# Kernel optimization log

Measured on AMD Instinct MI355X. Metric: run time of the kernel, lower is better.

The kernel has to match this reference:

```python
import jax, jax.numpy as jnp
import numpy as np

B, T, C = 16, 2048, 64  # n_embd = 64


def setup_inputs() -> dict:
    key = jax.random.key(0)
    ks = jax.random.split(key, 4)
    scale = 1.0 / np.sqrt(C)
    x = jax.random.normal(ks[0], (B, T, C), dtype=jnp.float32)
    Wk = jax.random.normal(ks[1], (C, C), dtype=jnp.float32) * scale
    Wq = jax.random.normal(ks[2], (C, C), dtype=jnp.float32) * scale
    Wv = jax.random.normal(ks[3], (C, C), dtype=jnp.float32) * scale
    bk = jnp.zeros((C,), dtype=jnp.float32)
    bq = jnp.zeros((C,), dtype=jnp.float32)
    bv = jnp.zeros((C,), dtype=jnp.float32)
    return {"x": x, "Wk": Wk, "bk": bk, "Wq": Wq, "bq": bq, "Wv": Wv, "bv": bv}


def reference(x, Wk, bk, Wq, bq, Wv, bv):
    # Faithful to source: wei = q @ k^T * C**0.5 (MULTIPLY, as in original code),
    # softmax over last axis, no causal mask (tril is built but unused), dropout=0.
    _, _, c = x.shape
    k = jnp.einsum('btc,cd->btd', x, Wk) + bk
    q = jnp.einsum('btc,cd->btd', x, Wq) + bq
    v = jnp.einsum('btc,cd->btd', x, Wv) + bv
    wei = jnp.einsum('btd,bsd->bts', q, k) * (c ** 0.5)  # [B,T,T]
    wei = jax.nn.softmax(wei, axis=-1)
    out = jnp.einsum('bts,bsd->btd', wei, v)  # [B,T,C]
    return out
```

## Files before the change

### kernel.cpp

```cpp
#include <hip/hip_runtime.h>
#include <hip/hip_bf16.h>
#include <stdint.h>

#define NBATCH 16
#define NT 2048
#define NC 64
#define QT 128
#define KT 128
#define SC_LOG2E 11.5415603f

typedef __bf16 bf16x8 __attribute__((ext_vector_type(8)));
typedef float f32x4 __attribute__((ext_vector_type(4)));
typedef float f32x16 __attribute__((ext_vector_type(16)));

#define Z16 {0.f,0.f,0.f,0.f,0.f,0.f,0.f,0.f,0.f,0.f,0.f,0.f,0.f,0.f,0.f,0.f}

extern "C" __device__ float __ocml_exp2_f32(float);

static __device__ __forceinline__ unsigned short f2bf(float f) {
  __bf16 h = (__bf16)f;
  union { __bf16 h; unsigned short u; } a; a.h = h; return a.u;
}
static __device__ __forceinline__ float bf2f(unsigned short h) {
  union { uint32_t u; float f; } a; a.u = ((uint32_t)h) << 16;
  return a.f;
}
static __device__ __forceinline__ float fasu(uint32_t u) {
  union { uint32_t u; float f; } a; a.u = u; return a.f;
}
static __device__ __forceinline__ uint32_t uasf(float f) {
  union { float f; uint32_t u; } a; a.f = f; return a.u;
}

#define GLD_LDS16(gsrc, ldst)                                                  \
  __builtin_amdgcn_global_load_lds(                                            \
      (const __attribute__((address_space(1))) void*)(gsrc),                   \
      (__attribute__((address_space(3))) void*)(ldst), 16, 0, 0)

__global__ __launch_bounds__(256, 2) void prep_w(
    const float* __restrict__ Wk, const float* __restrict__ Wq,
    const float* __restrict__ Wv,
    unsigned short* __restrict__ wt_hi, unsigned short* __restrict__ wt_lo)
{
  __shared__ unsigned short hbuf[64][66];
  __shared__ unsigned short lbuf[64][66];
  const int m = (int)blockIdx.x;
  const float* Wm = (m == 0) ? Wk : (m == 1 ? Wq : Wv);
  const int tid = (int)threadIdx.x;
  for (int idx = tid; idx < 1024; idx += 256) {
    int c = idx >> 4, o4 = (idx & 15) * 4;
    float4 v = *(const float4*)(Wm + c * 64 + o4);
    float vals[4] = {v.x, v.y, v.z, v.w};
#pragma unroll
    for (int j = 0; j < 4; ++j) {
      unsigned short h = f2bf(vals[j]);
      hbuf[o4 + j][c] = h;
      lbuf[o4 + j][c] = f2bf(vals[j] - bf2f(h));
    }
  }
  __syncthreads();
  for (int idx = tid; idx < 1024; idx += 256) {
    int o = idx >> 4, c0 = (idx & 15) * 4;
    ushort4 hv, lv;
    hv.x = hbuf[o][c0]; hv.y = hbuf[o][c0 + 1];
    hv.z = hbuf[o][c0 + 2]; hv.w = hbuf[o][c0 + 3];
    lv.x = lbuf[o][c0]; lv.y = lbuf[o][c0 + 1];
    lv.z = lbuf[o][c0 + 2]; lv.w = lbuf[o][c0 + 3];
    *(ushort4*)(wt_hi + (size_t)(m * 64 + o) * 64 + c0) = hv;
    *(ushort4*)(wt_lo + (size_t)(m * 64 + o) * 64 + c0) = lv;
  }
}

__global__ __launch_bounds__(256, 2) void proj_kernel(
    const float* __restrict__ x,
    const unsigned short* __restrict__ wt_hi, const unsigned short* __restrict__ wt_lo,
    const float* __restrict__ bk, const float* __restrict__ bq, const float* __restrict__ bv,
    unsigned short* __restrict__ khi, unsigned short* __restrict__ klo,
    unsigned short* __restrict__ qhi, unsigned short* __restrict__ qlo,
    unsigned short* __restrict__ vt)
{
  __shared__ __align__(16) char smem[65536];
  const int XH = 0, XL = 8192, WTH = 16384, WTL = 40960, VTB = 0;
  const int tid = (int)threadIdx.x;
  const int l = tid & 63, w = tid >> 6;
  const int lr = l & 15, lg = l >> 4;
  const int blk = (int)blockIdx.x;
  const int rowbase = blk * 64;
  const int bb = blk >> 5;

#pragma unroll
  for (int ch4 = 0; ch4 < 6; ++ch4) {
    int ch = ch4 * 4 + w;
    int d = ch * 1024 + l * 16;
    int swk = d ^ (((d >> 7) & 7) << 4);
    GLD_LDS16((const char*)wt_hi + swk, smem + WTH + ch * 1024);
    GLD_LDS16((const char*)wt_lo + swk, smem + WTL + ch * 1024);
  }
  for (int c = tid; c < 1024; c += 256) {
    int row = c >> 4, d0 = (c & 15) * 4;
    const float4 xv = *(const float4*)(x + (size_t)(rowbase + row) * NC + d0);
    unsigned short h0 = f2bf(xv.x), h1 = f2bf(xv.y), h2 = f2bf(xv.z), h3 = f2bf(xv.w);
    unsigned short m0 = f2bf(xv.x - bf2f(h0)), m1 = f2bf(xv.y - bf2f(h1));
    unsigned short m2 = f2bf(xv.z - bf2f(h2)), m3 = f2bf(xv.w - bf2f(h3));
    uint2 ph, pl;
    ph.x = (uint32_t)h0 | ((uint32_t)h1 << 16); ph.y = (uint32_t)h2 | ((uint32_t)h3 << 16);
    pl.x = (uint32_t)m0 | ((uint32_t)m1 << 16); pl.y = (uint32_t)m2 | ((uint32_t)m3 << 16);
    int byteoff = (row * 128 + d0 * 2) ^ ((row & 7) << 4);
    *(uint2*)(smem + XH + byteoff) = ph;
    *(uint2*)(smem + XL + byteoff) = pl;
  }
  __syncthreads();

  bf16x8 xh[2], xl[2];
  {
    int row = w * 16 + lr;
#pragma unroll
    for (int dc = 0; dc < 2; ++dc) {
      int byteoff = (row * 128 + (dc * 32 + lg * 8) * 2) ^ ((row & 7) << 4);
      xh[dc] = *(const bf16x8*)(smem + XH + byteoff);
      xl[dc] = *(const bf16x8*)(smem + XL + byteoff);
    }
  }
  f32x4 acc[12];
#pragma unroll
  for (int nb = 0; nb < 12; ++nb) {
    f32x4 a = {0.f, 0.f, 0.f, 0.f};
    int og = nb * 16 + lr;
#pragma unroll
    for (int dc = 0; dc < 2; ++dc) {
      int byteoff = (og * 128 + (dc * 32 + lg * 8) * 2) ^ ((og & 7) << 4);
      bf16x8 bh = *(const bf16x8*)(smem + WTH + byteoff);
      bf16x8 bl = *(const bf16x8*)(smem + WTL + byteoff);
      a = __builtin_amdgcn_mfma_f32_16x16x32_bf16(bh, xh[dc], a, 0, 0, 0);
      a = __builtin_amdgcn_mfma_f32_16x16x32_bf16(bl, xh[dc], a, 0, 0, 0);
      a = __builtin_amdgcn_mfma_f32_16x16x32_bf16(bh, xl[dc], a, 0, 0, 0);
    }
    acc[nb] = a;
  }
  __syncthreads();

  const int tloc = w * 16 + lr;
  const size_t gt = (size_t)(rowbase + tloc);
#pragma unroll
  for (int nb = 0; nb < 12; ++nb) {
    int ogb = (nb & 3) * 16 + lg * 4;
    const float* bp = (nb < 4) ? bk : (nb < 8 ? bq : bv);
    float4 bias = *(const float4*)(bp + ogb);
    float v0 = acc[nb][0] + bias.x, v1 = acc[nb][1] + bias.y,
          v2 = acc[nb][2] + bias.z, v3 = acc[nb][3] + bias.w;
    if (nb < 8) {
      if (nb >= 4) { v0 *= SC_LOG2E; v1 *= SC_LOG2E; v2 *= SC_LOG2E; v3 *= SC_LOG2E; }
      ushort4 hv, lv;
      hv.x = f2bf(v0); lv.x = f2bf(v0 - bf2f(hv.x));
      hv.y = f2bf(v1); lv.y = f2bf(v1 - bf2f(hv.y));
      hv.z = f2bf(v2); lv.z = f2bf(v2 - bf2f(hv.z));
      hv.w = f2bf(v3); lv.w = f2bf(v3 - bf2f(hv.w));
      unsigned short* dH = (nb < 4) ? khi : qhi;
      unsigned short* dL = (nb < 4) ? klo : qlo;
      *(ushort4*)(dH + gt * 64 + ogb) = hv;
      *(ushort4*)(dL + gt * 64 + ogb) = lv;
    } else {
      float vs[4] = {v0, v1, v2, v3};
#pragma unroll
      for (int r = 0; r < 4; ++r) {
        int o = ogb + r;
        int byteoff = (o * 128 + tloc * 2) ^ ((o & 7) << 4);
        *(unsigned short*)(smem + VTB + byteoff) = f2bf(vs[r]);
      }
    }
  }
  __syncthreads();
  for (int cc = tid; cc < 512; cc += 256) {
    int o = cc >> 3, t0 = (cc & 7) * 8;
    int byteoff = (o * 128 + t0 * 2) ^ ((o & 7) << 4);
    uint4 v = *(const uint4*)(smem + VTB + byteoff);
    *(uint4*)(vt + ((size_t)bb * 64 + o) * NT + (size_t)(blk & 31) * 64 + t0) = v;
  }
}

__global__ __launch_bounds__(1024, 4) void attn_kernel(
    const unsigned short* __restrict__ khi, const unsigned short* __restrict__ klo,
    const unsigned short* __restrict__ qhi, const unsigned short* __restrict__ qlo,
    const unsigned short* __restrict__ vt,
    float* __restrict__ out)
{
  __shared__ __align__(16) char smem[98304];
  const int BUF = 49152;
  const int MLB = 65536;
  const int tid = (int)threadIdx.x;
  const int l = tid & 63, w = tid >> 6;
  const int lq = l & 31;
  const bool hi = (l >= 32);
  const int hioff = hi ? 16 : 0;
  const int r = w & 3;
  const int cc = w >> 2;
  const int lb = ((int)(blockIdx.x & 7) << 5) | ((int)blockIdx.x >> 3);
  const int bb = lb >> 4;
  const int qt = lb & 15;

  const char* kh_base = (const char*)(khi + (size_t)bb * NT * 64);
  const char* kl_base = (const char*)(klo + (size_t)bb * NT * 64);
  const char* v_base  = (const char*)(vt + (size_t)bb * 64 * NT);

#define STAGE_TILE(bufp_, it_)                                                 \
  do {                                                                         \
    const char* kh_t = kh_base + (size_t)(it_) * 16384;                        \
    const char* kl_t = kl_base + (size_t)(it_) * 16384;                        \
    const char* v_tb = v_base + (size_t)(it_) * 256;                           \
    int d_ = w * 1024 + l * 16;                                                \
    int swk_ = d_ ^ (((d_ >> 7) & 7) << 4);                                    \
    GLD_LDS16(kh_t + swk_, (bufp_) + w * 1024);                                \
    GLD_LDS16(kl_t + swk_, (bufp_) + 16384 + w * 1024);                        \
    int o_ = d_ >> 8;                                                          \
    int swv_ = (d_ & 255) ^ ((o_ & 7) << 4);                                   \
    GLD_LDS16(v_tb + (size_t)o_ * 4096 + swv_, (bufp_) + 32768 + w * 1024);    \
  } while (0)

  STAGE_TILE(smem, 0);
  bf16x8 Qh[4], Ql[4];
  {
    const char* qh_t = (const char*)qhi + ((size_t)bb * NT + (size_t)qt * QT) * 128;
    const char* ql_t = (const char*)qlo + ((size_t)bb * NT + (size_t)qt * QT) * 128;
    int qrow = r * 32 + lq;
#pragma unroll
    for (int dc = 0; dc < 4; ++dc) {
      Qh[dc] = *(const bf16x8*)(qh_t + qrow * 128 + dc * 32 + hioff);
      Ql[dc] = *(const bf16x8*)(ql_t + qrow * 128 + dc * 32 + hioff);
    }
  }
  asm volatile("s_waitcnt vmcnt(0)" ::: "memory");
  __builtin_amdgcn_s_barrier();
  asm volatile("" ::: "memory");

  f32x16 O0 = Z16, O1 = Z16;
  float mrun = -1e30f, lrun = 0.f;
  const int swr = (lq & 7) << 4;

  for (int it = 0; it < NT / KT; ++it) {
    char* cb = smem + (it & 1) * BUF;
    if (it + 1 < NT / KT) STAGE_TILE(smem + ((it + 1) & 1) * BUF, it + 1);

    f32x16 S = Z16;
    __builtin_amdgcn_s_setprio(1);
#pragma unroll
    for (int dc = 0; dc < 4; ++dc) {
      int krow = cc * 32 + lq;
      int cchunk = (dc * 32 + hioff) ^ swr;
      bf16x8 Ah = *(const bf16x8*)(cb + krow * 128 + cchunk);
      bf16x8 Al = *(const bf16x8*)(cb + 16384 + krow * 128 + cchunk);
      S = __builtin_amdgcn_mfma_f32_32x32x16_bf16(Ah, Qh[dc], S, 0, 0, 0);
      S = __builtin_amdgcn_mfma_f32_32x32x16_bf16(Al, Qh[dc], S, 0, 0, 0);
      S = __builtin_amdgcn_mfma_f32_32x32x16_bf16(Ah, Ql[dc], S, 0, 0, 0);
    }
    __builtin_amdgcn_s_setprio(0);

    float m01 = fmaxf(S[0], S[1]),   m23 = fmaxf(S[2], S[3]);
    float m45 = fmaxf(S[4], S[5]),   m67 = fmaxf(S[6], S[7]);
    float m89 = fmaxf(S[8], S[9]),   mab = fmaxf(S[10], S[11]);
    float mcd = fmaxf(S[12], S[13]), mef = fmaxf(S[14], S[15]);
    float pmax = fmaxf(fmaxf(fmaxf(m01, m23), fmaxf(m45, m67)),
                       fmaxf(fmaxf(m89, mab), fmaxf(mcd, mef)));
    {
      auto sw = __builtin_amdgcn_permlane32_swap(uasf(pmax), uasf(pmax), false, false);
      pmax = fmaxf(fasu(sw[0]), fasu(sw[1]));
    }
    if (__any(pmax > mrun + 11.55f)) {
      float mnew = fmaxf(mrun, pmax);
      float alpha = __ocml_exp2_f32(mrun - mnew);
      O0 *= alpha; O1 *= alpha; lrun *= alpha; mrun = mnew;
    }
    float p[16];
#pragma unroll
    for (int i = 0; i < 16; ++i) p[i] = __ocml_exp2_f32(S[i] - mrun);
    float s01 = p[0] + p[1],   s23 = p[2] + p[3];
    float s45 = p[4] + p[5],   s67 = p[6] + p[7];
    float s89 = p[8] + p[9],   sab = p[10] + p[11];
    float scd = p[12] + p[13], sef = p[14] + p[15];
    float ts = ((s01 + s23) + (s45 + s67)) + ((s89 + sab) + (scd + sef));
    {
      auto sw = __builtin_amdgcn_permlane32_swap(uasf(ts), uasf(ts), false, false);
      ts = fasu(sw[0]) + fasu(sw[1]);
    }
    lrun += ts;

#define PV_CHUNK(kc_)                                                          \
    {                                                                          \
      const int b_ = 8 * (kc_);                                                \
      uint32_t X0, X1, Y0, Y1;                                                 \
      asm("v_cvt_pk_bf16_f32 %0, %1, %2" : "=v"(X0) : "v"(p[b_+0]), "v"(p[b_+1])); \
      asm("v_cvt_pk_bf16_f32 %0, %1, %2" : "=v"(X1) : "v"(p[b_+2]), "v"(p[b_+3])); \
      asm("v_cvt_pk_bf16_f32 %0, %1, %2" : "=v"(Y0) : "v"(p[b_+4]), "v"(p[b_+5])); \
      asm("v_cvt_pk_bf16_f32 %0, %1, %2" : "=v"(Y1) : "v"(p[b_+6]), "v"(p[b_+7])); \
      auto sw0 = __builtin_amdgcn_permlane32_swap(X0, Y0, false, false);       \
      auto sw1 = __builtin_amdgcn_permlane32_swap(X1, Y1, false, false);       \
      union { uint32_t u[4]; bf16x8 v; } cvb;                                  \
      cvb.u[0] = sw0[0]; cvb.u[1] = sw1[0];                                    \
      cvb.u[2] = sw0[1]; cvb.u[3] = sw1[1];                                    \
      bf16x8 Bp = cvb.v;                                                       \
      int vcol = 64 * cc + 32 * (kc_) + hioff;                                 \
      {                                                                        \
        bf16x8 Av = *(const bf16x8*)(cb + 32768 + lq * 256 + (vcol ^ swr));    \
        O0 = __builtin_amdgcn_mfma_f32_32x32x16_bf16(Av, Bp, O0, 0, 0, 0);     \
      }                                                                        \
      {                                                                        \
        bf16x8 Av = *(const bf16x8*)(cb + 32768 + (32 + lq) * 256 + (vcol ^ swr)); \
        O1 = __builtin_amdgcn_mfma_f32_32x32x16_bf16(Av, Bp, O1, 0, 0, 0);     \
      }                                                                        \
    }
    __builtin_amdgcn_s_setprio(1);
    PV_CHUNK(0)
    PV_CHUNK(1)
    __builtin_amdgcn_s_setprio(0);
#undef PV_CHUNK

    asm volatile("s_waitcnt vmcnt(0)" ::: "memory");
    __builtin_amdgcn_s_barrier();
    asm volatile("" ::: "memory");
    __builtin_amdgcn_sched_barrier(0);
  }

  const int lsw = (l & 7) << 4;
#define DUMP(idx_)                                                             \
  {                                                                            \
    char* dd = smem + (idx_) * 8192 + l * 128;                                 \
    _Pragma("unroll")                                                          \
    for (int g = 0; g < 4; ++g) {                                              \
      f32x4 t0, t1;                                                            \
      _Pragma("unroll")                                                        \
      for (int j = 0; j < 4; ++j) { t0[j] = O0[4*g+j]; t1[j] = O1[4*g+j]; }    \
      *(f32x4*)(dd + ((g * 16) ^ lsw)) = t0;                                   \
      *(f32x4*)(dd + ((64 + g * 16) ^ lsw)) = t1;                              \
    }                                                                          \
    *(float*)(smem + MLB + (idx_) * 256 + lq * 8) = mrun;                      \
    *(float*)(smem + MLB + (idx_) * 256 + lq * 8 + 4) = lrun;                  \
  }
#define MERGE(idx_)                                                            \
  {                                                                            \
    const char* ds = smem + (idx_) * 8192 + l * 128;                           \
    float m1 = *(const float*)(smem + MLB + (idx_) * 256 + lq * 8);            \
    float l1 = *(const float*)(smem + MLB + (idx_) * 256 + lq * 8 + 4);        \
    float M = fmaxf(mrun, m1);                                                 \
    float a0 = __ocml_exp2_f32(mrun - M);                                      \
    float a1 = __ocml_exp2_f32(m1 - M);                                        \
    lrun = lrun * a0 + l1 * a1;                                                \
    mrun = M;                                                                  \
    _Pragma("unroll")                                                          \
    for (int g = 0; g < 4; ++g) {                                              \
      f32x4 o1a = *(const f32x4*)(ds + ((g * 16) ^ lsw));                      \
      f32x4 o1b = *(const f32x4*)(ds + ((64 + g * 16) ^ lsw));                 \
      _Pragma("unroll")                                                        \
      for (int j = 0; j < 4; ++j) {                                            \
        O0[4*g+j] = O0[4*g+j] * a0 + o1a[j] * a1;                              \
        O1[4*g+j] = O1[4*g+j] * a0 + o1b[j] * a1;                              \
      }                                                                        \
    }                                                                          \
  }
  if (cc & 1) DUMP(r * 2 + (cc >> 1));
  __syncthreads();
  if (!(cc & 1)) MERGE(r * 2 + (cc >> 1));
  __syncthreads();
  if (cc == 2) DUMP(r * 2 + 1);
  __syncthreads();
  if (cc == 0) {
    MERGE(r * 2 + 1);
    float inv = 1.0f / lrun;
    float* orow = out + ((size_t)bb * NT + (size_t)qt * QT + r * 32 + lq) * 64;
#pragma unroll
    for (int g = 0; g < 4; ++g) {
      int d0 = 8 * g + (hi ? 4 : 0);
      f32x4 s0, s1;
#pragma unroll
      for (int j = 0; j < 4; ++j) { s0[j] = O0[4*g+j] * inv; s1[j] = O1[4*g+j] * inv; }
      *(f32x4*)(orow + d0) = s0;
      *(f32x4*)(orow + d0 + 32) = s1;
    }
  }
#undef DUMP
#undef MERGE
#undef STAGE_TILE
}

extern "C" void kernel_launch(void* const* d_in, const int* in_sizes, int n_in,
                              void* d_out, int out_size, void* d_ws, size_t ws_size,
                              hipStream_t stream) {
  const float* x  = (const float*)d_in[0];
  const float* Wk = (const float*)d_in[1];
  const float* bk = (const float*)d_in[2];
  const float* Wq = (const float*)d_in[3];
  const float* bq = (const float*)d_in[4];
  const float* Wv = (const float*)d_in[5];
  const float* bv = (const float*)d_in[6];
  float* out = (float*)d_out;

  const size_t NE = (size_t)NBATCH * NT * 64;
  unsigned short* ws = (unsigned short*)d_ws;
  unsigned short* khi = ws;
  unsigned short* klo = ws + NE;
  unsigned short* qhi = ws + 2 * NE;
  unsigned short* qlo = ws + 3 * NE;
  unsigned short* vt  = ws + 4 * NE;
  unsigned short* wt_hi = ws + 5 * NE;
  unsigned short* wt_lo = wt_hi + 192 * 64;

  prep_w<<<dim3(3), dim3(256), 0, stream>>>(Wk, Wq, Wv, wt_hi, wt_lo);
  proj_kernel<<<dim3((NBATCH * NT) / 64), dim3(256), 0, stream>>>(
      x, wt_hi, wt_lo, bk, bq, bv, khi, klo, qhi, qlo, vt);
  attn_kernel<<<dim3(NBATCH * (NT / QT)), dim3(1024), 0, stream>>>(
      khi, klo, qhi, qlo, vt, out);
}
```

Measured before the change: 72.79 us.

## Unroll attention loop by two with constant buffers and fold max into accumulator init

The attention main loop is unrolled by two so the double-buffer offsets become compile-time constants, and the prefetch guard disappears from the steady-state body. The running max is subtracted up front by initialising the score accumulator to -mrun, so the exp step skips a subtraction when no rescale is needed. The projection kernel now issues all x loads before the weight-to-LDS copies, giving them more time in flight. These changes trim per-iteration ALU and address work and raise memory-level parallelism, at the cost of larger code and more registers.

```diff
diff --git a/kernel.cpp b/kernel.cpp
--- a/kernel.cpp
+++ b/kernel.cpp
@@ -88,6 +88,13 @@
   const int rowbase = blk * 64;
   const int bb = blk >> 5;
 
+  float4 xv[4];
+#pragma unroll
+  for (int j = 0; j < 4; ++j) {
+    int c = tid + j * 256;
+    int row = c >> 4, d0 = (c & 15) * 4;
+    xv[j] = *(const float4*)(x + (size_t)(rowbase + row) * NC + d0);
+  }
 #pragma unroll
   for (int ch4 = 0; ch4 < 6; ++ch4) {
     int ch = ch4 * 4 + w;
@@ -96,12 +103,13 @@
     GLD_LDS16((const char*)wt_hi + swk, smem + WTH + ch * 1024);
     GLD_LDS16((const char*)wt_lo + swk, smem + WTL + ch * 1024);
   }
-  for (int c = tid; c < 1024; c += 256) {
+#pragma unroll
+  for (int j = 0; j < 4; ++j) {
+    int c = tid + j * 256;
     int row = c >> 4, d0 = (c & 15) * 4;
-    const float4 xv = *(const float4*)(x + (size_t)(rowbase + row) * NC + d0);
-    unsigned short h0 = f2bf(xv.x), h1 = f2bf(xv.y), h2 = f2bf(xv.z), h3 = f2bf(xv.w);
-    unsigned short m0 = f2bf(xv.x - bf2f(h0)), m1 = f2bf(xv.y - bf2f(h1));
-    unsigned short m2 = f2bf(xv.z - bf2f(h2)), m3 = f2bf(xv.w - bf2f(h3));
+    unsigned short h0 = f2bf(xv[j].x), h1 = f2bf(xv[j].y), h2 = f2bf(xv[j].z), h3 = f2bf(xv[j].w);
+    unsigned short m0 = f2bf(xv[j].x - bf2f(h0)), m1 = f2bf(xv[j].y - bf2f(h1));
+    unsigned short m2 = f2bf(xv[j].z - bf2f(h2)), m3 = f2bf(xv[j].w - bf2f(h3));
     uint2 ph, pl;
     ph.x = (uint32_t)h0 | ((uint32_t)h1 << 16); ph.y = (uint32_t)h2 | ((uint32_t)h3 << 16);
     pl.x = (uint32_t)m0 | ((uint32_t)m1 << 16); pl.y = (uint32_t)m2 | ((uint32_t)m3 << 16);
@@ -202,21 +210,21 @@
   const char* kl_base = (const char*)(klo + (size_t)bb * NT * 64);
   const char* v_base  = (const char*)(vt + (size_t)bb * 64 * NT);
 
-#define STAGE_TILE(bufp_, it_)                                                 \
+#define STAGE_TILE(bufoff_, it_)                                               \
   do {                                                                         \
     const char* kh_t = kh_base + (size_t)(it_) * 16384;                        \
     const char* kl_t = kl_base + (size_t)(it_) * 16384;                        \
     const char* v_tb = v_base + (size_t)(it_) * 256;                           \
     int d_ = w * 1024 + l * 16;                                                \
     int swk_ = d_ ^ (((d_ >> 7) & 7) << 4);                                    \
-    GLD_LDS16(kh_t + swk_, (bufp_) + w * 1024);                                \
-    GLD_LDS16(kl_t + swk_, (bufp_) + 16384 + w * 1024);                        \
+    GLD_LDS16(kh_t + swk_, smem + (bufoff_) + w * 1024);                       \
+    GLD_LDS16(kl_t + swk_, smem + (bufoff_) + 16384 + w * 1024);               \
     int o_ = d_ >> 8;                                                          \
     int swv_ = (d_ & 255) ^ ((o_ & 7) << 4);                                   \
-    GLD_LDS16(v_tb + (size_t)o_ * 4096 + swv_, (bufp_) + 32768 + w * 1024);    \
+    GLD_LDS16(v_tb + (size_t)o_ * 4096 + swv_, smem + (bufoff_) + 32768 + w * 1024); \
   } while (0)
 
-  STAGE_TILE(smem, 0);
+  STAGE_TILE(0, 0);
   bf16x8 Qh[4], Ql[4];
   {
     const char* qh_t = (const char*)qhi + ((size_t)bb * NT + (size_t)qt * QT) * 128;
@@ -233,59 +241,66 @@
   asm volatile("" ::: "memory");
 
   f32x16 O0 = Z16, O1 = Z16;
-  float mrun = -1e30f, lrun = 0.f;
+  float mrun = 0.f, lrun = 0.f;
   const int swr = (lq & 7) << 4;
 
-  for (int it = 0; it < NT / KT; ++it) {
-    char* cb = smem + (it & 1) * BUF;
-    if (it + 1 < NT / KT) STAGE_TILE(smem + ((it + 1) & 1) * BUF, it + 1);
-
-    f32x16 S = Z16;
-    __builtin_amdgcn_s_setprio(1);
-#pragma unroll
-    for (int dc = 0; dc < 4; ++dc) {
-      int krow = cc * 32 + lq;
-      int cchunk = (dc * 32 + hioff) ^ swr;
-      bf16x8 Ah = *(const bf16x8*)(cb + krow * 128 + cchunk);
-      bf16x8 Al = *(const bf16x8*)(cb + 16384 + krow * 128 + cchunk);
-      S = __builtin_amdgcn_mfma_f32_32x32x16_bf16(Ah, Qh[dc], S, 0, 0, 0);
-      S = __builtin_amdgcn_mfma_f32_32x32x16_bf16(Al, Qh[dc], S, 0, 0, 0);
-      S = __builtin_amdgcn_mfma_f32_32x32x16_bf16(Ah, Ql[dc], S, 0, 0, 0);
-    }
-    __builtin_amdgcn_s_setprio(0);
-
-    float m01 = fmaxf(S[0], S[1]),   m23 = fmaxf(S[2], S[3]);
-    float m45 = fmaxf(S[4], S[5]),   m67 = fmaxf(S[6], S[7]);
-    float m89 = fmaxf(S[8], S[9]),   mab = fmaxf(S[10], S[11]);
-    float mcd = fmaxf(S[12], S[13]), mef = fmaxf(S[14], S[15]);
-    float pmax = fmaxf(fmaxf(fmaxf(m01, m23), fmaxf(m45, m67)),
-                       fmaxf(fmaxf(m89, mab), fmaxf(mcd, mef)));
-    {
-      auto sw = __builtin_amdgcn_permlane32_swap(uasf(pmax), uasf(pmax), false, false);
-      pmax = fmaxf(fasu(sw[0]), fasu(sw[1]));
-    }
-    if (__any(pmax > mrun + 11.55f)) {
-      float mnew = fmaxf(mrun, pmax);
-      float alpha = __ocml_exp2_f32(mrun - mnew);
-      O0 *= alpha; O1 *= alpha; lrun *= alpha; mrun = mnew;
-    }
-    float p[16];
-#pragma unroll
-    for (int i = 0; i < 16; ++i) p[i] = __ocml_exp2_f32(S[i] - mrun);
-    float s01 = p[0] + p[1],   s23 = p[2] + p[3];
-    float s45 = p[4] + p[5],   s67 = p[6] + p[7];
-    float s89 = p[8] + p[9],   sab = p[10] + p[11];
-    float scd = p[12] + p[13], sef = p[14] + p[15];
-    float ts = ((s01 + s23) + (s45 + s67)) + ((s89 + sab) + (scd + sef));
-    {
-      auto sw = __builtin_amdgcn_permlane32_swap(uasf(ts), uasf(ts), false, false);
-      ts = fasu(sw[0]) + fasu(sw[1]);
-    }
-    lrun += ts;
-
-#define PV_CHUNK(kc_)                                                          \
+#define BODY(it_, CB_, NB_, STG_)                                              \
+  {                                                                            \
+    if (STG_) STAGE_TILE(NB_, (it_) + 1);                                      \
+       \
+    f32x16 S;                                                                  \
+    _Pragma("unroll")                                                          \
+    for (int i = 0; i < 16; ++i) S[i] = -mrun;                                 \
+    __builtin_amdgcn_s_setprio(1);                                             \
+    _Pragma("unroll")                                                          \
+    for (int dc = 0; dc < 4; ++dc) {                                           \
+      int krow = cc * 32 + lq;                                                 \
+      int cchunk = (dc * 32 + hioff) ^ swr;                                    \
+      bf16x8 Ah = *(const bf16x8*)(smem + (CB_) + krow * 128 + cchunk);        \
+      bf16x8 Al = *(const bf16x8*)(smem + (CB_) + 16384 + krow * 128 + cchunk);\
+      S = __builtin_amdgcn_mfma_f32_32x32x16_bf16(Ah, Qh[dc], S, 0, 0, 0);     \
+      S = __builtin_amdgcn_mfma_f32_32x32x16_bf16(Al, Qh[dc], S, 0, 0, 0);     \
+      S = __builtin_amdgcn_mfma_f32_32x32x16_bf16(Ah, Ql[dc], S, 0, 0, 0);     \
+    }                                                                          \
+    __builtin_amdgcn_s_setprio(0);                                             \
+                     \
+    float t0 = fmaxf(fmaxf(S[0], S[1]), S[2]);                                 \
+    float t1 = fmaxf(fmaxf(S[3], S[4]), S[5]);                                 \
+    float t2 = fmaxf(fmaxf(S[6], S[7]), S[8]);                                 \
+    float t3 = fmaxf(fmaxf(S[9], S[10]), S[11]);                               \
+    float t4 = fmaxf(fmaxf(S[12], S[13]), S[14]);                              \
+    float pmax = fmaxf(fmaxf(fmaxf(t0, t1), t2), fmaxf(fmaxf(t3, t4), S[15])); \
     {                                                                          \
-      const int b_ = 8 * (kc_);                                                \
+      auto sw = __builtin_amdgcn_permlane32_swap(uasf(pmax), uasf(pmax), false, false); \
+      pmax = fmaxf(fasu(sw[0]), fasu(sw[1]));                                  \
+    }                                                                          \
+    float p[16];                                                               \
+    if (__any(pmax > 11.55f)) {                                                \
+      float d = fmaxf(pmax, 0.f);                                              \
+      mrun += d;                                                               \
+      float alpha = __ocml_exp2_f32(-d);                                       \
+      O0 *= alpha; O1 *= alpha; lrun *= alpha;                                 \
+      _Pragma("unroll")                                                        \
+      for (int i = 0; i < 16; ++i) p[i] = __ocml_exp2_f32(S[i] - d);           \
+    } else {                                                                   \
+      _Pragma("unroll")                                                        \
+      for (int i = 0; i < 16; ++i) p[i] = __ocml_exp2_f32(S[i]);               \
+    }                                                                          \
+    float s01 = p[0] + p[1],   s23 = p[2] + p[3];                              \
+    float s45 = p[4] + p[5],   s67 = p[6] + p[7];                              \
+    float s89 = p[8] + p[9],   sab = p[10] + p[11];                            \
+    float scd = p[12] + p[13], sef = p[14] + p[15];                            \
+    float ts = ((s01 + s23) + (s45 + s67)) + ((s89 + sab) + (scd + sef));      \
+    {                                                                          \
+      auto sw = __builtin_amdgcn_permlane32_swap(uasf(ts), uasf(ts), false, false); \
+      ts = fasu(sw[0]) + fasu(sw[1]);                                          \
+    }                                                                          \
+    lrun += ts;                                                                \
+                                                         \
+    __builtin_amdgcn_s_setprio(1);                                             \
+    _Pragma("unroll")                                                          \
+    for (int kc = 0; kc < 2; ++kc) {                                           \
+      const int b_ = 8 * kc;                                                   \
       uint32_t X0, X1, Y0, Y1;                                                 \
       asm("v_cvt_pk_bf16_f32 %0, %1, %2" : "=v"(X0) : "v"(p[b_+0]), "v"(p[b_+1])); \
       asm("v_cvt_pk_bf16_f32 %0, %1, %2" : "=v"(X1) : "v"(p[b_+2]), "v"(p[b_+3])); \
@@ -297,27 +312,26 @@
       cvb.u[0] = sw0[0]; cvb.u[1] = sw1[0];                                    \
       cvb.u[2] = sw0[1]; cvb.u[3] = sw1[1];                                    \
       bf16x8 Bp = cvb.v;                                                       \
-      int vcol = 64 * cc + 32 * (kc_) + hioff;                                 \
-      {                                                                        \
-        bf16x8 Av = *(const bf16x8*)(cb + 32768 + lq * 256 + (vcol ^ swr));    \
-        O0 = __builtin_amdgcn_mfma_f32_32x32x16_bf16(Av, Bp, O0, 0, 0, 0);     \
-      }                                                                        \
-      {                                                                        \
-        bf16x8 Av = *(const bf16x8*)(cb + 32768 + (32 + lq) * 256 + (vcol ^ swr)); \
-        O1 = __builtin_amdgcn_mfma_f32_32x32x16_bf16(Av, Bp, O1, 0, 0, 0);     \
-      }                                                                        \
-    }
-    __builtin_amdgcn_s_setprio(1);
-    PV_CHUNK(0)
-    PV_CHUNK(1)
-    __builtin_amdgcn_s_setprio(0);
-#undef PV_CHUNK
-
-    asm volatile("s_waitcnt vmcnt(0)" ::: "memory");
-    __builtin_amdgcn_s_barrier();
-    asm volatile("" ::: "memory");
-    __builtin_amdgcn_sched_barrier(0);
-  }
+      int vcol = 64 * cc + 32 * kc + hioff;                                    \
+      bf16x8 Av0 = *(const bf16x8*)(smem + (CB_) + 32768 + lq * 256 + (vcol ^ swr)); \
+      bf16x8 Av1 = *(const bf16x8*)(smem + (CB_) + 32768 + (32 + lq) * 256 + (vcol ^ swr)); \
+      O0 = __builtin_amdgcn_mfma_f32_32x32x16_bf16(Av0, Bp, O0, 0, 0, 0);      \
+      O1 = __builtin_amdgcn_mfma_f32_32x32x16_bf16(Av1, Bp, O1, 0, 0, 0);      \
+    }                                                                          \
+    __builtin_amdgcn_s_setprio(0);                                             \
+    asm volatile("s_waitcnt vmcnt(0)" ::: "memory");                           \
+    __builtin_amdgcn_s_barrier();                                              \
+    asm volatile("" ::: "memory");                                             \
+    __builtin_amdgcn_sched_barrier(0);                                         \
+  }
+
+#pragma unroll 1
+  for (int i2 = 0; i2 < 7; ++i2) {
+    BODY(2 * i2,     0,   BUF, 1)
+    BODY(2 * i2 + 1, BUF, 0,   1)
+  }
+  BODY(14, 0,   BUF, 1)
+  BODY(15, BUF, 0,   0)
 
   const int lsw = (l & 7) << 4;
 #define DUMP(idx_)                                                             \
@@ -377,6 +391,7 @@
   }
 #undef DUMP
 #undef MERGE
+#undef BODY
 #undef STAGE_TILE
 }
 
```

New measurement: 152.7 us. 2.1x slower.
